# Kernel tuning notes

Hardware: AMD Instinct MI355X
Metric: run time of the kernel (lower is better)

## Reference

```python
import jax, jax.numpy as jnp
import numpy as np

N_NODES = 100000
N_EDGES = 1600000
D_EDGE = 50
D_NODE = 8


def setup_inputs() -> dict:
    key = jax.random.key(0)
    k1, k2, k3 = jax.random.split(key, 3)
    nodes = jax.random.normal(k1, (N_NODES, D_NODE), dtype=jnp.float32)
    edges = jax.random.normal(k2, (N_EDGES, D_EDGE), dtype=jnp.float32)
    receivers = jax.random.randint(k3, (N_EDGES,), 0, N_NODES, dtype=jnp.int64)
    return {"nodes": nodes, "edges": edges, "receivers": receivers}


def reference(nodes, edges, receivers):
    # torch: zeros(num_nodes, d_edge).index_add(0, receivers, edges)
    num_nodes = nodes.shape[0]
    return jax.ops.segment_sum(edges, receivers, num_segments=num_nodes)
```

## Files before the change

kernel.cpp:

```cpp
#include <hip/hip_runtime.h>


#define N_EDGES   1600000
#define N_GROUPS  (N_EDGES / 4)
#define D_EDGE    50
#define N_NODES   100000

#define NBUCK     256
#define NPB_C     391
#define NREPK     4
#define QCAP      1920
#define GPB       512
#define LCAP1     28
#define NSLICE    16
#define SLICE_N   25
#define LCAP2     120
#define CNT_STRIDE 16

#define BCNT_OFF  0u
#define BIDS_OFF  65536u
#define WS_NEEDED (65536u + 7864320u)

__device__ __forceinline__ int clamp_node(int r) {
    return (r < 0) ? 0 : ((r >= N_NODES) ? N_NODES - 1 : r);
}

__global__ __launch_bounds__(256, 4) void bucket_scatter_kernel(
    const int* __restrict__ receivers, int* __restrict__ bcnt, int* __restrict__ bids)
{
    __shared__ int s_list[NBUCK][LCAP1];
    __shared__ int s_cnt[NBUCK];

    const int t   = threadIdx.x;
    const int b   = blockIdx.x;
    const int rep = b & (NREPK - 1);

    s_cnt[t] = 0;
    __syncthreads();

    const int gbase = b * GPB;
    #pragma unroll
    for (int g = 0; g < GPB / 256; ++g) {
        int idx = gbase + g * 256 + t;
        if (idx < N_GROUPS) {
            int4 rv = ((const int4*)receivers)[idx];
            int e = idx * 4;
#define BIN1(comp, k)                                                       \
            {                                                               \
                int r   = clamp_node(rv.comp);                              \
                int bkt = r / NPB_C;                                        \
                int lr  = r - bkt * NPB_C;                                  \
                int v   = ((e + k) << 9) | lr;                              \
                int p   = atomicAdd(&s_cnt[bkt], 1);                        \
                if (p < LCAP1) {                                            \
                    s_list[bkt][p] = v;                                     \
                } else {             \
                    int q = atomicAdd(&bcnt[(bkt * NREPK + rep) * CNT_STRIDE], 1); \
                    if ((unsigned)q < QCAP) bids[(bkt * NREPK + rep) * QCAP + q] = v; \
                }                                                           \
            }
            BIN1(x, 0) BIN1(y, 1) BIN1(z, 2) BIN1(w, 3)
#undef BIN1
        }
    }
    __syncthreads();

    int n = s_cnt[t];
    n = (n > LCAP1) ? LCAP1 : n;
    if (n > 0) {
        int base = atomicAdd(&bcnt[(t * NREPK + rep) * CNT_STRIDE], n);
        int* dst = bids + (t * NREPK + rep) * QCAP;
        for (int i = 0; i < n; ++i) {
            int q = base + i;
            if ((unsigned)q < QCAP) dst[q] = s_list[t][i];
        }
    }
}

__global__ __launch_bounds__(256, 8) void bucket_gather_kernel(
    const float* __restrict__ edges, const int* __restrict__ bcnt,
    const int* __restrict__ bids, float* __restrict__ out)
{
    __shared__ int s_list[SLICE_N][LCAP2];
    __shared__ int s_lcnt[SLICE_N];

    const int blk  = blockIdx.x;
    const int bkt  = blk >> 4;
    const int sl   = blk & (NSLICE - 1);
    const int t    = threadIdx.x;
    const int wid  = t >> 6;
    const int lane = t & 63;
    const int l    = (lane < D_EDGE) ? lane : 0;

    if (t < SLICE_N) s_lcnt[t] = 0;
    __syncthreads();

    const int lo = sl * SLICE_N;
    const int hi = lo + SLICE_N;

    #pragma unroll
    for (int rep = 0; rep < NREPK; ++rep) {
        int cnt = bcnt[(bkt * NREPK + rep) * CNT_STRIDE];
        cnt = (cnt < 0) ? 0 : ((cnt > QCAP) ? QCAP : cnt);
        const int* seg = bids + (bkt * NREPK + rep) * QCAP;
        for (int i = t; i < cnt; i += 256) {
            int v  = seg[i];
            int lr = v & 511;
            if (lr >= lo && lr < hi) {
                int e = (int)((unsigned)v >> 9);
                e = (e >= N_EDGES) ? 0 : e;
                int p = atomicAdd(&s_lcnt[lr - lo], 1);
                if (p < LCAP2) s_list[lr - lo][p] = e;
            }
        }
    }
    __syncthreads();

    for (int ln = wid; ln < SLICE_N; ln += 4) {
        int lrf = lo + ln;
        if (lrf >= NPB_C) continue;
        int node = bkt * NPB_C + lrf;
        if (node >= N_NODES) continue;
        int deg = s_lcnt[ln];
        deg = (deg > LCAP2) ? LCAP2 : deg;
        float acc = 0.0f;

#define G16(k) \
        int   e##k = s_list[ln][(j + k < deg) ? (j + k) : 0]; \
        float m##k = (j + k < deg) ? 1.0f : 0.0f; \
        float a##k = edges[e##k * D_EDGE + l];

        for (int j = 0; j < deg; j += 16) {
            G16(0)  G16(1)  G16(2)  G16(3)
            G16(4)  G16(5)  G16(6)  G16(7)
            G16(8)  G16(9)  G16(10) G16(11)
            G16(12) G16(13) G16(14) G16(15)
            acc += (((m0 * a0 + m1 * a1) + (m2 * a2 + m3 * a3))
                  + ((m4 * a4 + m5 * a5) + (m6 * a6 + m7 * a7)))
                 + (((m8 * a8 + m9 * a9) + (m10 * a10 + m11 * a11))
                  + ((m12 * a12 + m13 * a13) + (m14 * a14 + m15 * a15)));
        }
#undef G16

        if (lane < D_EDGE) out[node * D_EDGE + lane] = acc;
    }
}

__global__ __launch_bounds__(256) void scatter_add_kernel(
    const float* __restrict__ edges, const int* __restrict__ receivers,
    float* __restrict__ out)
{
    long long t = (long long)blockIdx.x * blockDim.x + threadIdx.x;
    if (t >= (long long)N_EDGES * D_EDGE) return;
    int e = (int)(t / D_EDGE);
    int d = (int)(t - (long long)e * D_EDGE);
    int r = receivers[e];
    r = clamp_node(r);
    atomicAdd(&out[(long long)r * D_EDGE + d], edges[t]);
}

extern "C" void kernel_launch(void* const* d_in, const int* in_sizes, int n_in,
                              void* d_out, int out_size, void* d_ws, size_t ws_size,
                              hipStream_t stream) {
    const float* edges     = (const float*)d_in[1];
    const int*   receivers = (const int*)d_in[2];
    float*       out       = (float*)d_out;

    if (ws_size < WS_NEEDED || d_ws == nullptr) {
        hipMemsetAsync(d_out, 0, (size_t)out_size * sizeof(float), stream);
        const long long total = (long long)N_EDGES * D_EDGE;
        const int grid = (int)((total + 255) / 256);
        scatter_add_kernel<<<grid, 256, 0, stream>>>(edges, receivers, out);
        return;
    }

    char* ws   = (char*)d_ws;
    int*  bcnt = (int*)(ws + BCNT_OFF);
    int*  bids = (int*)(ws + BIDS_OFF);

    hipMemsetAsync(bcnt, 0, NBUCK * NREPK * CNT_STRIDE * sizeof(int), stream);

    const int g1 = (N_GROUPS + GPB - 1) / GPB;
    bucket_scatter_kernel<<<g1, 256, 0, stream>>>(receivers, bcnt, bids);

    bucket_gather_kernel<<<NBUCK * NSLICE, 256, 0, stream>>>(edges, bcnt, bids, out);
}
```

Baseline: 471.5 us.

## Replace per-node gather with LDS atomic accumulation over wider bucket slices

The gather kernel now splits each bucket into 4 slices of 98 nodes instead of 16 slices of 25. Each block compacts its matching edge ids with a wavefront ballot into one flat list and streams edge rows into a shared float accumulator using LDS atomics. This cuts the 16x re-read of each bucket's id lists and removes the per-node degree-padded loops. The cost is LDS atomic contention, lower occupancy, and edges silently dropped if a slice exceeds ECAP entries.

```diff
diff --git a/kernel.cpp b/kernel.cpp
--- a/kernel.cpp
+++ b/kernel.cpp
@@ -12,9 +12,10 @@
 #define QCAP      1920
 #define GPB       512
 #define LCAP1     28
-#define NSLICE    16
-#define SLICE_N   25
-#define LCAP2     120
+#define NSLICE    4
+#define SLICE_N   98
+#define PADW      51
+#define ECAP      2048
 #define CNT_STRIDE 16
 
 #define BCNT_OFF  0u
@@ -77,22 +78,24 @@
     }
 }
 
-__global__ __launch_bounds__(256, 8) void bucket_gather_kernel(
+__global__ __launch_bounds__(256, 4) void slice_accum_kernel(
     const float* __restrict__ edges, const int* __restrict__ bcnt,
     const int* __restrict__ bids, float* __restrict__ out)
 {
-    __shared__ int s_list[SLICE_N][LCAP2];
-    __shared__ int s_lcnt[SLICE_N];
+    __shared__ float s_acc[SLICE_N][PADW];
+    __shared__ int   s_edge[ECAP];
+    __shared__ int   s_n;
 
     const int blk  = blockIdx.x;
-    const int bkt  = blk >> 4;
+    const int bkt  = blk >> 2;
     const int sl   = blk & (NSLICE - 1);
     const int t    = threadIdx.x;
+    const int lane = t & 63;
     const int wid  = t >> 6;
-    const int lane = t & 63;
     const int l    = (lane < D_EDGE) ? lane : 0;
 
-    if (t < SLICE_N) s_lcnt[t] = 0;
+    for (int i = t; i < SLICE_N * PADW; i += 256) ((float*)s_acc)[i] = 0.0f;
+    if (t == 0) s_n = 0;
     __syncthreads();
 
     const int lo = sl * SLICE_N;
@@ -103,46 +106,60 @@
         int cnt = bcnt[(bkt * NREPK + rep) * CNT_STRIDE];
         cnt = (cnt < 0) ? 0 : ((cnt > QCAP) ? QCAP : cnt);
         const int* seg = bids + (bkt * NREPK + rep) * QCAP;
-        for (int i = t; i < cnt; i += 256) {
-            int v  = seg[i];
+        int cnt_up = (cnt + 255) & ~255;
+        for (int i = t; i < cnt_up; i += 256) {
+            bool valid = (i < cnt);
+            int v  = valid ? seg[i] : 0;
             int lr = v & 511;
-            if (lr >= lo && lr < hi) {
-                int e = (int)((unsigned)v >> 9);
-                e = (e >= N_EDGES) ? 0 : e;
-                int p = atomicAdd(&s_lcnt[lr - lo], 1);
-                if (p < LCAP2) s_list[lr - lo][p] = e;
+            bool match = valid && (lr >= lo) && (lr < hi);
+            unsigned long long m = __ballot(match);
+            int cw = __popcll(m);
+            if (cw) {
+                int basew = 0;
+                if (lane == 0) basew = atomicAdd(&s_n, cw);
+                basew = __shfl(basew, 0);
+                if (match) {
+                    int pre = __popcll(m & ((1ull << lane) - 1ull));
+                    int p = basew + pre;
+                    if (p < ECAP) s_edge[p] = v;
+                }
             }
         }
     }
     __syncthreads();
 
-    for (int ln = wid; ln < SLICE_N; ln += 4) {
+    int n = s_n;
+    n = (n > ECAP) ? ECAP : n;
+
+    for (int bi = wid * 8; bi < n; bi += 32) {
+        float a[8]; int lr8[8]; bool ok[8];
+        #pragma unroll
+        for (int k = 0; k < 8; ++k) {
+            int idx = bi + k;
+            bool o = (idx < n);
+            int v = o ? s_edge[idx] : 0;
+            int e = (int)((unsigned)v >> 9);
+            e = (e >= N_EDGES) ? 0 : e;
+            int r = (v & 511) - lo;
+            r = (r < 0) ? 0 : ((r >= SLICE_N) ? SLICE_N - 1 : r);
+            lr8[k] = r; ok[k] = o;
+            a[k] = edges[(long long)e * D_EDGE + l];
+        }
+        #pragma unroll
+        for (int k = 0; k < 8; ++k) {
+            if (ok[k] && lane < D_EDGE) atomicAdd(&s_acc[lr8[k]][l], a[k]);
+        }
+    }
+    __syncthreads();
+
+    for (int i = t; i < SLICE_N * D_EDGE; i += 256) {
+        int ln = i / D_EDGE;
+        int d  = i - ln * D_EDGE;
         int lrf = lo + ln;
         if (lrf >= NPB_C) continue;
         int node = bkt * NPB_C + lrf;
         if (node >= N_NODES) continue;
-        int deg = s_lcnt[ln];
-        deg = (deg > LCAP2) ? LCAP2 : deg;
-        float acc = 0.0f;
-
-#define G16(k) \
-        int   e##k = s_list[ln][(j + k < deg) ? (j + k) : 0]; \
-        float m##k = (j + k < deg) ? 1.0f : 0.0f; \
-        float a##k = edges[e##k * D_EDGE + l];
-
-        for (int j = 0; j < deg; j += 16) {
-            G16(0)  G16(1)  G16(2)  G16(3)
-            G16(4)  G16(5)  G16(6)  G16(7)
-            G16(8)  G16(9)  G16(10) G16(11)
-            G16(12) G16(13) G16(14) G16(15)
-            acc += (((m0 * a0 + m1 * a1) + (m2 * a2 + m3 * a3))
-                  + ((m4 * a4 + m5 * a5) + (m6 * a6 + m7 * a7)))
-                 + (((m8 * a8 + m9 * a9) + (m10 * a10 + m11 * a11))
-                  + ((m12 * a12 + m13 * a13) + (m14 * a14 + m15 * a15)));
-        }
-#undef G16
-
-        if (lane < D_EDGE) out[node * D_EDGE + lane] = acc;
+        out[node * D_EDGE + d] = s_acc[ln][d];
     }
 }
 
@@ -183,5 +200,5 @@
     const int g1 = (N_GROUPS + GPB - 1) / GPB;
     bucket_scatter_kernel<<<g1, 256, 0, stream>>>(receivers, bcnt, bids);
 
-    bucket_gather_kernel<<<NBUCK * NSLICE, 256, 0, stream>>>(edges, bcnt, bids, out);
-}
+    slice_accum_kernel<<<NBUCK * NSLICE, 256, 0, stream>>>(edges, bcnt, bids, out);
+}
```

Result: slower. 785.2 us (+66.5%).
